# Performance work log

Hardware: AMD Instinct MI355X
Metric: run time of the kernel (lower is better)

## Reference

```python
import jax, jax.numpy as jnp
import numpy as np


def setup_inputs() -> dict:
    key = jax.random.key(0)
    # batch of 1D signals; DST is applied along the last dimension
    x = jax.random.normal(key, (16384, 1024), dtype=jnp.float32)
    return {"x": x}


def reference(x):
    # DST-II: y_k = sum_{n=0}^{N-1} x_n * sin(pi/N * (n + 1/2) * (k + 1))
    # (The original docstring says 'cos' but the op is a discrete SINE transform;
    #  the DREAMPlace kernel computes the DST-II above via FFT-style tricks.)
    N = x.shape[-1]
    n = jnp.arange(N, dtype=x.dtype)
    k = jnp.arange(N, dtype=x.dtype)
    # [N, N] sine basis: rows indexed by n (input), cols by k (output)
    S = jnp.sin((jnp.pi / N) * (n[:, None] + 0.5) * (k[None, :] + 1.0))
    # batched transform over leading dims
    lead = x.shape[:-1]
    y = jnp.einsum('bn,nk->bk', x.reshape(-1, N), S)
    return y.reshape(*lead, N)
```

## Files before the change

kernel.cpp:

```cpp
#include <hip/hip_runtime.h>
#include <cstdint>


static constexpr int BR4[16] = {0, 8, 4, 12, 2, 10, 6, 14,
                                1, 9, 5, 13, 3, 11, 7, 15};
static constexpr float W16C[8] = {1.0f, 0.9238795325f, 0.7071067812f,
                                  0.3826834324f, 0.0f, -0.3826834324f,
                                  -0.7071067812f, -0.9238795325f};
static constexpr float W16S[8] = {-0.0f, -0.3826834324f, -0.7071067812f,
                                  -0.9238795325f, -1.0f, -0.9238795325f,
                                  -0.7071067812f, -0.3826834324f};

__device__ __forceinline__ float sinr(float r) {
  return __builtin_amdgcn_sinf(r);
}
__device__ __forceinline__ float cosr(float r) {
  float t = r + 0.25f;
  t -= (t >= 1.0f) ? 1.0f : 0.0f;
  return __builtin_amdgcn_sinf(t);
}

__device__ __forceinline__ void twmul(int tw, float xr, float xi,
                                      float& yr, float& yi) {
  if (tw == 0) {
    yr = xr; yi = xi;
  } else if (tw == 4) {
    yr = xi; yi = -xr;
  } else if (tw == 2) {
    yr = 0.70710678118f * (xr + xi);
    yi = 0.70710678118f * (xi - xr);
  } else if (tw == 6) {
    yr = 0.70710678118f * (xi - xr);
    yi = -0.70710678118f * (xr + xi);
  } else {
    yr = xr * W16C[tw] - xi * W16S[tw];
    yi = xr * W16S[tw] + xi * W16C[tw];
  }
}

__global__ __launch_bounds__(256, 3) void dst_fft(const float* __restrict__ X,
                                                  float* __restrict__ Y) {
  __shared__ __align__(16) float lds_all[4][64 * 16];

  const int t = threadIdx.x;
  const int l = t & 63;
  const int w = t >> 6;
  float* lds = &lds_all[w][0];
  const int row = blockIdx.x * 4 + w;

  const int c = l & 3;
  const int m2l = l >> 2;
  const int e = ((c & 1) << 1) | (c >> 1);
  const int sstar = (int)(__brev((unsigned)m2l) >> 28);
  const int pl = sstar >> 3;
  const int ccs = (sstar >> 1) & 3;
  const int subo = (sstar & 1) * 2;

  const float* xr = X + (size_t)row * 1024;

  float re[16], im[16], odd[8];
#pragma unroll
  for (int j = 0; j < 8; ++j) {
    float2 v = *(const float2*)(xr + 2 * l + 128 * j);
    re[j] = v.x;
    odd[j] = v.y;
  }
#pragma unroll
  for (int j = 0; j < 8; ++j)
    re[15 - j] = -__shfl_xor(odd[j], 63);

#pragma unroll
  for (int o = 0; o < 8; ++o) {
    float d = re[o] - re[o + 8];
    re[o] += re[o + 8];
    im[o] = 0.0f;
    if (o == 0) {
      re[8] = d;            im[8] = 0.0f;
    } else if (o == 4) {
      re[12] = 0.0f;        im[12] = -d;
    } else {
      re[o + 8] = d * W16C[o];
      im[o + 8] = d * W16S[o];
    }
  }
#pragma unroll
  for (int H = 4; H >= 1; H >>= 1) {
#pragma unroll
    for (int b = 0; b < 16; b += 2 * H) {
#pragma unroll
      for (int o = 0; o < H; ++o) {
        int i0 = b + o, i1 = i0 + H;
        float ar = re[i0] - re[i1], ai = im[i0] - im[i1];
        re[i0] += re[i1];
        im[i0] += im[i1];
        twmul(o * (8 / H), ar, ai, re[i1], im[i1]);
      }
    }
  }

  {
    float rb = (float)l * (1.0f / 1024.0f);
    float wr = cosr(rb), wi = -sinr(rb);
    float cr = wr, ci = wi;
#pragma unroll
    for (int m2 = 1; m2 < 16; ++m2) {
      if (m2 > 1) {
        float nr = cr * wr - ci * wi;
        ci = cr * wi + ci * wr;
        cr = nr;
      }
      int i = BR4[m2];
      float tr = re[i] * cr - im[i] * ci;
      im[i] = re[i] * ci + im[i] * cr;
      re[i] = tr;
    }
  }

  float re2[16], im2[16];
#pragma unroll
  for (int p = 0; p < 2; ++p) {
    if (p)
      __asm__ volatile("s_waitcnt lgkmcnt(0)" ::: "memory");
#pragma unroll
    for (int cc = 0; cc < 4; ++cc) {
      int ch = 4 * p + cc;
      float4 v = make_float4(re[2 * ch], im[2 * ch],
                             re[2 * ch + 1], im[2 * ch + 1]);
      *(float4*)(lds + l * 16 + ((cc ^ ((l >> 1) & 3)) & 3) * 4) = v;
    }
    __asm__ volatile("s_waitcnt lgkmcnt(0)" ::: "memory");
    if (pl == p) {
#pragma unroll
      for (int i = 0; i < 16; ++i) {
        int r = c + 4 * BR4[i];
        int q = (ccs ^ ((r >> 1) & 3)) & 3;
        float2 v = *(const float2*)(lds + r * 16 + q * 4 + subo);
        re2[i] = v.x;
        im2[i] = v.y;
      }
    }
  }

#pragma unroll
  for (int H = 1; H <= 8; H <<= 1) {
#pragma unroll
    for (int b = 0; b < 16; b += 2 * H) {
#pragma unroll
      for (int o = 0; o < H; ++o) {
        int i0 = b + o, i1 = i0 + H;
        float tr, ti;
        twmul(o * (8 / H), re2[i1], im2[i1], tr, ti);
        re2[i1] = re2[i0] - tr;
        im2[i1] = im2[i0] - ti;
        re2[i0] += tr;
        im2[i0] += ti;
      }
    }
  }

  {
    float rb = (float)c * (1.0f / 64.0f);
    float br = cosr(rb), bi = -sinr(rb);
    float cr = br, ci = bi;
#pragma unroll
    for (int m = 1; m < 16; ++m) {
      if (m > 1) {
        float nr = cr * br - ci * bi;
        ci = cr * bi + ci * br;
        cr = nr;
      }
      float tr = re2[m] * cr - im2[m] * ci;
      im2[m] = re2[m] * ci + im2[m] * cr;
      re2[m] = tr;
    }
  }

  {
    const float sgA = (c & 2) ? -1.0f : 1.0f;
    const bool rot = (c == 3);
    const float sgB = (c & 1) ? -1.0f : 1.0f;
#pragma unroll
    for (int i = 0; i < 16; ++i) {
      float tr = __shfl_xor(re2[i], 2), ti = __shfl_xor(im2[i], 2);
      float ar = tr + sgA * re2[i], ai = ti + sgA * im2[i];
      float br = rot ? ai : ar;
      float bi = rot ? -ar : ai;
      tr = __shfl_xor(br, 1);
      ti = __shfl_xor(bi, 1);
      re2[i] = tr + sgB * br;
      im2[i] = ti + sgB * bi;
    }
  }

  {
    const float DC = 0.99969881869620422f;
    const float DS = 0.02454122852291229f;
    float r0 = (float)(m2l + 256 * e) * (1.0f / 4096.0f);
    float pc = cosr(r0), ps = sinr(r0);
    float* yr = Y + (size_t)row * 1024 + (1023 - m2l - 256 * e);
#pragma unroll
    for (int s2 = 0; s2 < 16; ++s2) {
      yr[-16 * s2] = re2[s2] * pc + im2[s2] * ps;
      if (s2 < 15) {
        float nc = pc * DC - ps * DS;
        ps = ps * DC + pc * DS;
        pc = nc;
      }
    }
  }
}

extern "C" void kernel_launch(void* const* d_in, const int* in_sizes, int n_in,
                              void* d_out, int out_size, void* d_ws, size_t ws_size,
                              hipStream_t stream) {
  const float* X = (const float*)d_in[0];
  float* Y = (float*)d_out;
  dst_fft<<<dim3(4096), dim3(256), 0, stream>>>(X, Y);
}
```

Before: 118.5 us.

## Pack two real rows into one complex FFT per wavefront

Each wavefront now transforms two rows at once, putting one row's reordered data in the real part and the other's in the imaginary part of a single complex FFT. The two spectra are then separated with the Hermitian-symmetry trick, using cross-lane shuffles before the twiddled outputs are written. This halves the FFT arithmetic and the number of wavefronts per row, so the grid is halved and the occupancy hint drops from 3 to 2. In exchange it adds more shuffle traffic, more live registers and lower occupancy.

```diff
diff --git a/kernel.cpp b/kernel.cpp
--- a/kernel.cpp
+++ b/kernel.cpp
@@ -38,7 +38,7 @@
   }
 }
 
-__global__ __launch_bounds__(256, 3) void dst_fft(const float* __restrict__ X,
+__global__ __launch_bounds__(256, 2) void dst_fft(const float* __restrict__ X,
                                                   float* __restrict__ Y) {
   __shared__ __align__(16) float lds_all[4][64 * 16];
 
@@ -46,7 +46,8 @@
   const int l = t & 63;
   const int w = t >> 6;
   float* lds = &lds_all[w][0];
-  const int row = blockIdx.x * 4 + w;
+  const int wid = blockIdx.x * 4 + w;
+  const int rowA = wid * 2;
 
   const int c = l & 3;
   const int m2l = l >> 2;
@@ -56,35 +57,29 @@
   const int ccs = (sstar >> 1) & 3;
   const int subo = (sstar & 1) * 2;
 
-  const float* xr = X + (size_t)row * 1024;
-
-  float re[16], im[16], odd[8];
-#pragma unroll
-  for (int j = 0; j < 8; ++j) {
-    float2 v = *(const float2*)(xr + 2 * l + 128 * j);
-    re[j] = v.x;
-    odd[j] = v.y;
-  }
+  const int Lp = (3 - c) + 4 * ((16 - m2l) & 15);
+  const int Lp0 = (c < 2) ? c : (5 - c);
+
+  const float* xa = X + (size_t)rowA * 1024;
+  float2 la[8], lb[8];
+#pragma unroll
+  for (int j = 0; j < 8; ++j) la[j] = *(const float2*)(xa + 2 * l + 128 * j);
 #pragma unroll
   for (int j = 0; j < 8; ++j)
-    re[15 - j] = -__shfl_xor(odd[j], 63);
-
-#pragma unroll
-  for (int o = 0; o < 8; ++o) {
-    float d = re[o] - re[o + 8];
-    re[o] += re[o + 8];
-    im[o] = 0.0f;
-    if (o == 0) {
-      re[8] = d;            im[8] = 0.0f;
-    } else if (o == 4) {
-      re[12] = 0.0f;        im[12] = -d;
-    } else {
-      re[o + 8] = d * W16C[o];
-      im[o + 8] = d * W16S[o];
-    }
-  }
-#pragma unroll
-  for (int H = 4; H >= 1; H >>= 1) {
+    lb[j] = *(const float2*)(xa + 1024 + 2 * l + 128 * j);
+
+  float re[16], im[16];
+#pragma unroll
+  for (int j = 0; j < 8; ++j) re[j] = la[j].x;
+#pragma unroll
+  for (int j = 0; j < 8; ++j) re[15 - j] = -__shfl_xor(la[j].y, 63);
+#pragma unroll
+  for (int j = 0; j < 8; ++j) im[j] = lb[j].x;
+#pragma unroll
+  for (int j = 0; j < 8; ++j) im[15 - j] = -__shfl_xor(lb[j].y, 63);
+
+#pragma unroll
+  for (int H = 8; H >= 1; H >>= 1) {
 #pragma unroll
     for (int b = 0; b < 16; b += 2 * H) {
 #pragma unroll
@@ -192,21 +187,44 @@
     }
   }
 
-  {
-    const float DC = 0.99969881869620422f;
-    const float DS = 0.02454122852291229f;
+  const float DC = 0.99969881869620422f;
+  const float DS = 0.02454122852291229f;
+  {
     float r0 = (float)(m2l + 256 * e) * (1.0f / 4096.0f);
-    float pc = cosr(r0), ps = sinr(r0);
-    float* yr = Y + (size_t)row * 1024 + (1023 - m2l - 256 * e);
+    float hpc = 0.5f * cosr(r0), hps = 0.5f * sinr(r0);
 #pragma unroll
     for (int s2 = 0; s2 < 16; ++s2) {
-      yr[-16 * s2] = re2[s2] * pc + im2[s2] * ps;
+      float A = re2[s2] * hpc + im2[s2] * hps;
+      float B = re2[s2] * hps - im2[s2] * hpc;
+      re2[s2] = A;
+      im2[s2] = B;
       if (s2 < 15) {
-        float nc = pc * DC - ps * DS;
-        ps = ps * DC + pc * DS;
-        pc = nc;
-      }
-    }
+        float nc = hpc * DC - hps * DS;
+        hps = hps * DC + hpc * DS;
+        hpc = nc;
+      }
+    }
+  }
+
+  float* ya = Y + (size_t)rowA * 1024 + (1023 - m2l - 256 * e);
+  float* yb = ya + 1024;
+#pragma unroll
+  for (int s2 = 0; s2 < 16; ++s2) {
+    const int r1 = (15 - s2) & 15;
+    const int r2 = (16 - s2) & 15;
+    const int lane2 = (s2 == 0) ? Lp0 : Lp;
+    float QA1 = __shfl(re2[r1], Lp), QB1 = __shfl(im2[r1], Lp);
+    float QA2 = __shfl(re2[r2], lane2), QB2 = __shfl(im2[r2], lane2);
+    float QA = (m2l == 0) ? QA2 : QA1;
+    float QB = (m2l == 0) ? QB2 : QB1;
+    float oa = re2[s2] + QB;
+    float ob = QA - im2[s2];
+    if (s2 == 0) {
+      oa = (l == 0) ? re2[0] + re2[0] : oa;
+      ob = (l == 0) ? -(im2[0] + im2[0]) : ob;
+    }
+    ya[-16 * s2] = oa;
+    yb[-16 * s2] = ob;
   }
 }
 
@@ -215,5 +233,5 @@
                               hipStream_t stream) {
   const float* X = (const float*)d_in[0];
   float* Y = (float*)d_out;
-  dst_fft<<<dim3(4096), dim3(256), 0, stream>>>(X, Y);
-}
+  dst_fft<<<dim3(2048), dim3(256), 0, stream>>>(X, Y);
+}
```

Measured after the change: 114.5 us. -3.4%, faster.
